# Performance work log

Hardware: AMD Instinct MI355X
Metric: run time of the kernel (lower is better)

## Reference

```python
import jax, jax.numpy as jnp
import numpy as np

D_MODEL = 1024
N_HEADS = 16
HEAD_DIM = D_MODEL // N_HEADS
D_FF = 4096
ROPE_BASE = 10000.0
LN_EPS = 1e-5


def setup_inputs() -> dict:
    key = jax.random.key(0)
    ks = jax.random.split(key, 12)
    B, S = 2, 2048
    s = 0.02
    inp = {
        "x": jax.random.normal(ks[0], (B, S, D_MODEL), dtype=jnp.float32),
        "Wq": jax.random.normal(ks[1], (D_MODEL, D_MODEL), dtype=jnp.float32) * s,
        "bq": jnp.zeros((D_MODEL,), jnp.float32),
        "Wk": jax.random.normal(ks[2], (D_MODEL, D_MODEL), dtype=jnp.float32) * s,
        "bk": jnp.zeros((D_MODEL,), jnp.float32),
        "Wv": jax.random.normal(ks[3], (D_MODEL, D_MODEL), dtype=jnp.float32) * s,
        "bv": jnp.zeros((D_MODEL,), jnp.float32),
        "Wo": jax.random.normal(ks[4], (D_MODEL, D_MODEL), dtype=jnp.float32) * s,
        "bo": jnp.zeros((D_MODEL,), jnp.float32),
        "ln1_g": jnp.ones((D_MODEL,), jnp.float32),
        "ln1_b": jnp.zeros((D_MODEL,), jnp.float32),
        "W1": jax.random.normal(ks[5], (D_MODEL, D_FF), dtype=jnp.float32) * s,
        "b1": jnp.zeros((D_FF,), jnp.float32),
        "W2": jax.random.normal(ks[6], (D_FF, D_MODEL), dtype=jnp.float32) * s,
        "b2": jnp.zeros((D_MODEL,), jnp.float32),
        "ln2_g": jnp.ones((D_MODEL,), jnp.float32),
        "ln2_b": jnp.zeros((D_MODEL,), jnp.float32),
    }
    return inp


def _layernorm(x, g, b):
    mu = jnp.mean(x, axis=-1, keepdims=True)
    var = jnp.var(x, axis=-1, keepdims=True)
    return (x - mu) * jax.lax.rsqrt(var + LN_EPS) * g + b


def _rope_cos_sin(seq_len, dtype):
    inv_freq = 1.0 / (ROPE_BASE ** (jnp.arange(0, HEAD_DIM, 2, dtype=jnp.float32) / HEAD_DIM))
    t = jnp.arange(seq_len, dtype=jnp.float32)
    freqs = jnp.einsum("i,j->ij", t, inv_freq)          # [S, HEAD_DIM/2]
    emb = jnp.concatenate([freqs, freqs], axis=-1)        # [S, HEAD_DIM]
    return jnp.cos(emb).astype(dtype), jnp.sin(emb).astype(dtype)


def _rotate_half(x):
    x1, x2 = jnp.split(x, 2, axis=-1)
    return jnp.concatenate([-x2, x1], axis=-1)


def reference(x, Wq, bq, Wk, bk, Wv, bv, Wo, bo, ln1_g, ln1_b,
              W1, b1, W2, b2, ln2_g, ln2_b):
    B, S, _ = x.shape
    residual = x
    h = _layernorm(x, ln1_g, ln1_b)

    def split_heads(y):  # [B,S,D] -> [B,H,S,hd]
        return y.reshape(B, S, N_HEADS, HEAD_DIM).transpose(0, 2, 1, 3)

    q = split_heads(h @ Wq + bq)
    k = split_heads(h @ Wk + bk)
    v = split_heads(h @ Wv + bv)

    cos, sin = _rope_cos_sin(S, x.dtype)  # [S, hd], broadcast over B,H
    q = q * cos + _rotate_half(q) * sin
    k = k * cos + _rotate_half(k) * sin

    scale = HEAD_DIM ** -0.5
    scores = jnp.einsum("bhqd,bhkd->bhqk", q, k) * scale
    attn = jax.nn.softmax(scores, axis=-1)
    ctx = jnp.einsum("bhqk,bhkd->bhqd", attn, v)           # [B,H,S,hd]
    ctx = ctx.transpose(0, 2, 1, 3).reshape(B, S, D_MODEL)
    attn_out = ctx @ Wo + bo

    x = residual + attn_out
    residual = x
    h = _layernorm(x, ln2_g, ln2_b)
    ffn = jax.nn.gelu(h @ W1 + b1, approximate=False) @ W2 + b2
    return residual + ffn
```

## Files before the change

kernel.cpp:

```cpp
#include <hip/hip_runtime.h>
#include <hip/hip_bf16.h>
#include <stdint.h>

#define S_LEN 2048
#define NH 16
#define HD 64
#define DM 1024
#define DFF 4096
#define MTOK 4096

typedef __attribute__((ext_vector_type(8))) short short8;
typedef __attribute__((ext_vector_type(4))) float f32x4;
typedef __attribute__((ext_vector_type(16))) float f32x16;
typedef __attribute__((ext_vector_type(2))) int i32x2;
typedef unsigned short u16;
typedef unsigned int u32;

__device__ __forceinline__ float bf2f(u16 u) {
  union { u32 i; float f; } x; x.i = ((u32)u) << 16; return x.f;
}
__device__ __forceinline__ u16 f2bf(float f) {
  union { float f; u32 i; } x; x.f = f;
  u32 r = x.i + 0x7fffu + ((x.i >> 16) & 1u);
  return (u16)(r >> 16);
}
__device__ __forceinline__ void gload16(const u16* g, u16* l) {
  __builtin_amdgcn_global_load_lds(
      (__attribute__((address_space(1))) u32*)g,
      (__attribute__((address_space(3))) u32*)l, 16, 0, 0);
}

#define VM0 asm volatile("s_waitcnt vmcnt(0)" ::: "memory")
#define VM6 asm volatile("s_waitcnt vmcnt(6)" ::: "memory")
#define BARR do { __builtin_amdgcn_s_barrier(); asm volatile("" ::: "memory"); } while (0)
#define LGKM0 do { asm volatile("s_waitcnt lgkmcnt(0)" ::: "memory"); __builtin_amdgcn_sched_barrier(0); } while (0)
#define PRIO1 __builtin_amdgcn_s_setprio(1)
#define PRIO0 __builtin_amdgcn_s_setprio(0)

__device__ __forceinline__ void transpose_tile(const float* __restrict__ W,
                                               u16* __restrict__ Wt, int K, int N,
                                               int n0, int k0, int tx, int ty,
                                               float (*tile)[33]) {
#pragma unroll
  for (int i = 0; i < 4; ++i)
    tile[ty + i * 8][tx] = W[(size_t)(k0 + ty + i * 8) * N + n0 + tx];
  __syncthreads();
#pragma unroll
  for (int i = 0; i < 4; ++i)
    Wt[(size_t)(n0 + ty + i * 8) * K + k0 + tx] = f2bf(tile[tx][ty + i * 8]);
}

__global__ __launch_bounds__(256) void prep(
    const float* __restrict__ Wq, const float* __restrict__ Wk,
    const float* __restrict__ Wv, const float* __restrict__ Wo,
    const float* __restrict__ W1, const float* __restrict__ W2,
    u16* __restrict__ WQKVT, u16* __restrict__ WOT, u16* __restrict__ W1T,
    u16* __restrict__ W2T, float* __restrict__ cosT, float* __restrict__ sinT,
    const float* __restrict__ x, const float* __restrict__ g,
    const float* __restrict__ b, u16* __restrict__ H) {
  __shared__ float tile[32][33];
  __shared__ float red[8];
  const int r = blockIdx.x;
  const int t = threadIdx.x;
  const int tx = t & 31, ty = t >> 5;
  if (r < 4096) {
    const float* W = (r < 1024) ? Wq : (r < 2048) ? Wk : (r < 3072) ? Wv : Wo;
    u16* Wt = (r < 1024) ? WQKVT
              : (r < 2048) ? WQKVT + 1024 * 1024
              : (r < 3072) ? WQKVT + 2 * 1024 * 1024 : WOT;
    int sub = r & 1023;
    transpose_tile(W, Wt, 1024, 1024, (sub & 31) * 32, (sub >> 5) * 32, tx, ty, tile);
  } else if (r < 8192) {
    int sub = r - 4096;
    transpose_tile(W1, W1T, 1024, 4096, (sub & 127) * 32, (sub >> 7) * 32, tx, ty, tile);
  } else if (r < 12288) {
    int sub = r - 8192;
    transpose_tile(W2, W2T, 4096, 1024, (sub & 31) * 32, (sub >> 5) * 32, tx, ty, tile);
  } else if (r < 12544) {
    int id = (r - 12288) * 256 + t;
    int s = id >> 5, j = id & 31;
    float inv = powf(10000.0f, -(float)j * (1.0f / 32.0f));
    float fr = (float)s * inv;
    cosT[id] = cosf(fr);
    sinT[id] = sinf(fr);
  } else {
    int row = r - 12544;
    float4 v = ((const float4*)(x + ((size_t)row << 10)))[t];
    float s = v.x + v.y + v.z + v.w;
    float q = v.x * v.x + v.y * v.y + v.z * v.z + v.w * v.w;
#pragma unroll
    for (int m = 1; m < 64; m <<= 1) {
      s += __shfl_xor(s, m, 64);
      q += __shfl_xor(q, m, 64);
    }
    int lane = t & 63, w = t >> 6;
    if (lane == 0) { red[w] = s; red[4 + w] = q; }
    __syncthreads();
    s = red[0] + red[1] + red[2] + red[3];
    q = red[4] + red[5] + red[6] + red[7];
    float mu = s * (1.0f / 1024.0f);
    float var = q * (1.0f / 1024.0f) - mu * mu;
    float rstd = rsqrtf(var + 1e-5f);
    float4 gv = ((const float4*)g)[t];
    float4 bv = ((const float4*)b)[t];
    ushort4 o;
    o.x = f2bf((v.x - mu) * rstd * gv.x + bv.x);
    o.y = f2bf((v.y - mu) * rstd * gv.y + bv.y);
    o.z = f2bf((v.z - mu) * rstd * gv.z + bv.z);
    o.w = f2bf((v.w - mu) * rstd * gv.w + bv.w);
    ((ushort4*)(H + ((size_t)row << 10)))[t] = o;
  }
}

__global__ __launch_bounds__(256) void ln_bf16(const float* __restrict__ x,
                                               const float* __restrict__ g,
                                               const float* __restrict__ b,
                                               u16* __restrict__ out) {
  int row = blockIdx.x;
  int t = threadIdx.x;
  float4 v = ((const float4*)(x + ((size_t)row << 10)))[t];
  float s = v.x + v.y + v.z + v.w;
  float q = v.x * v.x + v.y * v.y + v.z * v.z + v.w * v.w;
#pragma unroll
  for (int m = 1; m < 64; m <<= 1) {
    s += __shfl_xor(s, m, 64);
    q += __shfl_xor(q, m, 64);
  }
  __shared__ float red[8];
  int lane = t & 63, w = t >> 6;
  if (lane == 0) { red[w] = s; red[4 + w] = q; }
  __syncthreads();
  s = red[0] + red[1] + red[2] + red[3];
  q = red[4] + red[5] + red[6] + red[7];
  float mu = s * (1.0f / 1024.0f);
  float var = q * (1.0f / 1024.0f) - mu * mu;
  float rstd = rsqrtf(var + 1e-5f);
  float4 gv = ((const float4*)g)[t];
  float4 bv = ((const float4*)b)[t];
  ushort4 o;
  o.x = f2bf((v.x - mu) * rstd * gv.x + bv.x);
  o.y = f2bf((v.y - mu) * rstd * gv.y + bv.y);
  o.z = f2bf((v.z - mu) * rstd * gv.z + bv.z);
  o.w = f2bf((v.w - mu) * rstd * gv.w + bv.w);
  ((ushort4*)(out + ((size_t)row << 10)))[t] = o;
}

#define MMQ(IB, NB)                                                          \
  _Pragma("unroll") for (int i_ = 0; i_ < 4; ++i_)                           \
  _Pragma("unroll") for (int n_ = 0; n_ < 2; ++n_)                           \
  _Pragma("unroll") for (int k_ = 0; k_ < 2; ++k_)                           \
    acc[(IB) + i_][(NB) + n_] = __builtin_amdgcn_mfma_f32_16x16x32_bf16(     \
        a[i_][k_], b[(NB) + n_][k_], acc[(IB) + i_][(NB) + n_], 0, 0, 0);

template <int EPI>
__global__ __launch_bounds__(512, 2) void gemm256(
    const u16* __restrict__ A, const u16* __restrict__ Bt, int N, int K,
    const float* __restrict__ bias, const float* __restrict__ bq,
    const float* __restrict__ bk, const float* __restrict__ bv,
    const float* __restrict__ cosT, const float* __restrict__ sinT,
    u16* __restrict__ d0, u16* __restrict__ d1, u16* __restrict__ d2) {
  __shared__ __align__(16) u16 As[2][256 * 64];
  __shared__ __align__(16) u16 Bs[2][256 * 64];
  const int t = threadIdx.x;
  const int lane = t & 63, wid = t >> 6;
  const int fr = lane & 15, fq = lane >> 4;
  const int m0 = blockIdx.y << 8, n0 = blockIdx.x << 8;
  const int wmo = (wid >> 2) << 7;
  const int wno = (wid & 3) << 6;
  const int r7 = fr & 7;
  const int srow = t >> 3, ssl = t & 7;

  f32x4 acc[8][4];
#pragma unroll
  for (int i = 0; i < 8; ++i)
#pragma unroll
    for (int n = 0; n < 4; ++n) acc[i][n] = (f32x4){0.f, 0.f, 0.f, 0.f};

  short8 a[4][2], b[4][2];

  auto stageA = [&](int slot, int kt) {
#pragma unroll
    for (int c = 0; c < 4; ++c) {
      const int row = (c << 6) + srow;
      gload16(A + (size_t)(m0 + row) * K + kt + ((ssl ^ (row & 7)) << 3),
              &As[slot][(size_t)((c << 9) + t) << 3]);
    }
  };
  auto stageB = [&](int slot, int kt) {
#pragma unroll
    for (int c = 0; c < 4; ++c) {
      const int row = (c << 6) + srow;
      gload16(Bt + (size_t)(n0 + row) * K + kt + ((ssl ^ (row & 7)) << 3),
              &Bs[slot][(size_t)((c << 9) + t) << 3]);
    }
  };
  auto readA = [&](int slot, int ibase) {
#pragma unroll
    for (int i = 0; i < 4; ++i) {
      const u16* rp = &As[slot][(wmo + ((ibase + i) << 4) + fr) << 6];
      a[i][0] = *(const short8*)(rp + ((fq ^ r7) << 3));
      a[i][1] = *(const short8*)(rp + (((4 + fq) ^ r7) << 3));
    }
  };
  auto readB = [&](int slot, int nbase) {
#pragma unroll
    for (int n = 0; n < 2; ++n) {
      const u16* rp = &Bs[slot][(wno + ((nbase + n) << 4) + fr) << 6];
      b[nbase + n][0] = *(const short8*)(rp + ((fq ^ r7) << 3));
      b[nbase + n][1] = *(const short8*)(rp + (((4 + fq) ^ r7) << 3));
    }
  };

  stageA(0, 0);
  stageB(0, 0);
  const int iters = K >> 7;
  for (int it = 0; it < iters; ++it) {
    const int kt = it << 7;
    VM0; BARR;
    readA(0, 0); readB(0, 0);
    stageA(1, kt + 64);
    LGKM0; PRIO1; MMQ(0, 0); PRIO0;
    BARR;
    readB(0, 2);
    stageB(1, kt + 64);
    LGKM0; PRIO1; MMQ(0, 2); PRIO0;
    BARR;
    readA(0, 4);
    LGKM0; PRIO1; MMQ(4, 2); PRIO0;
    BARR;
    PRIO1; MMQ(4, 0); PRIO0;
    VM0; BARR;
    readA(1, 0); readB(1, 0);
    if (it + 1 < iters) stageA(0, kt + 128);
    LGKM0; PRIO1; MMQ(0, 0); PRIO0;
    BARR;
    readB(1, 2);
    if (it + 1 < iters) stageB(0, kt + 128);
    LGKM0; PRIO1; MMQ(0, 2); PRIO0;
    BARR;
    readA(1, 4);
    LGKM0; PRIO1; MMQ(4, 2); PRIO0;
    BARR;
    PRIO1; MMQ(4, 0); PRIO0;
  }

  if (EPI == 0) {
    const int colbase = n0 + wno;
    const int slice = colbase >> 10;
    const int cb = colbase & 1023;
    const int hh = cb >> 6;
    if (slice < 2) {
      const float sc = (slice == 0) ? 0.125f * 1.44269504088896f : 1.0f;
      const float* bb_ = (slice == 0) ? bq : bk;
      u16* dst = (slice == 0) ? d0 : d1;
#pragma unroll
      for (int i = 0; i < 8; ++i) {
        const int row0 = m0 + wmo + (i << 4) + (fq << 2);
#pragma unroll
        for (int n = 0; n < 2; ++n) {
          const int d = n * 16 + fr;
          const float blo = bb_[cb + d];
          const float bhi = bb_[cb + d + 32];
#pragma unroll
          for (int j = 0; j < 4; ++j) {
            const int row = row0 + j;
            const int ss = row & 2047, bb2 = row >> 11;
            const float c = cosT[ss * 32 + d];
            const float sn = sinT[ss * 32 + d];
            const float av = acc[i][n][j] + blo;
            const float bv2 = acc[i][n + 2][j] + bhi;
            const size_t base = ((size_t)((bb2 * 16 + hh) * 2048 + ss)) << 6;
            dst[base + d] = f2bf((av * c - bv2 * sn) * sc);
            dst[base + d + 32] = f2bf((bv2 * c + av * sn) * sc);
          }
        }
      }
    } else {
#pragma unroll
      for (int i = 0; i < 8; ++i) {
        const int row0 = m0 + wmo + (i << 4) + (fq << 2);
#pragma unroll
        for (int n = 0; n < 4; ++n) {
          const int d = n * 16 + fr;
          const float bia = bv[cb + d];
#pragma unroll
          for (int j = 0; j < 4; ++j) {
            const int row = row0 + j;
            const int ss = row & 2047, bb2 = row >> 11;
            d2[((size_t)((bb2 * 16 + hh) * 64 + d)) * 2048 + ss] =
                f2bf(acc[i][n][j] + bia);
          }
        }
      }
    }
  } else {
#pragma unroll
    for (int i = 0; i < 8; ++i) {
      const int row0 = m0 + wmo + (i << 4) + (fq << 2);
#pragma unroll
      for (int n = 0; n < 4; ++n) {
        const int col = n0 + wno + n * 16 + fr;
        const float bia = bias[col];
#pragma unroll
        for (int j = 0; j < 4; ++j) {
          const int row = row0 + j;
          const float v = acc[i][n][j] + bia;
          const float gl = 0.5f * v * (1.0f + erff(v * 0.70710678118f));
          d0[(size_t)row * N + col] = f2bf(gl);
        }
      }
    }
  }
}

__global__ __launch_bounds__(256, 2) void gemm_bt2(
    const u16* __restrict__ A, const u16* __restrict__ Bt, int K,
    const float* __restrict__ bias, const float* __restrict__ resid,
    float* __restrict__ dst) {
  __shared__ __align__(16) u16 As[3][128 * 64];
  __shared__ __align__(16) u16 Bs[3][64 * 64];
  const int t = threadIdx.x, lane = t & 63, wid = t >> 6;
  const int fr = lane & 15, fq = lane >> 4;
  const int bid = blockIdx.x;
  const int xcd = bid & 7, within = bid >> 3;
  const int m0 = (xcd * 4 + (within >> 4)) << 7;
  const int n0 = (within & 15) << 6;
  const int wm = (wid >> 1) << 6;
  const int wn = (wid & 1) << 5;
  const int sr = t >> 3, sl = t & 7;
  const int sw7 = fr & 7;

  f32x4 acc[4][2];
#pragma unroll
  for (int i = 0; i < 4; ++i)
#pragma unroll
    for (int n = 0; n < 2; ++n) acc[i][n] = (f32x4){0.f, 0.f, 0.f, 0.f};

  auto stage = [&](int b, int kt) {
#pragma unroll
    for (int c = 0; c < 4; ++c) {
      int R = c * 32 + sr;
      gload16(A + (size_t)(m0 + R) * K + kt + ((sl ^ (R & 7)) << 3),
              &As[b][R * 64 + sl * 8]);
    }
#pragma unroll
    for (int c = 0; c < 2; ++c) {
      int R = c * 32 + sr;
      gload16(Bt + (size_t)(n0 + R) * K + kt + ((sl ^ (R & 7)) << 3),
              &Bs[b][R * 64 + sl * 8]);
    }
  };

  stage(0, 0);
  stage(1, 64);
  const int iters = K >> 6;
  for (int it = 0; it < iters; ++it) {
    if (it + 1 < iters) { VM6; } else { VM0; }
    BARR;
    if (it + 2 < iters) stage((it + 2) % 3, (it + 2) << 6);
    const int slot = it % 3;
    short8 a[4][2], b[2][2];
#pragma unroll
    for (int i = 0; i < 4; ++i) {
      const char* rp = (const char*)&As[slot][(wm + i * 16 + fr) * 64];
      a[i][0] = *(const short8*)(rp + ((fq ^ sw7) << 4));
      a[i][1] = *(const short8*)(rp + (((4 + fq) ^ sw7) << 4));
    }
#pragma unroll
    for (int n = 0; n < 2; ++n) {
      const char* rp = (const char*)&Bs[slot][(wn + n * 16 + fr) * 64];
      b[n][0] = *(const short8*)(rp + ((fq ^ sw7) << 4));
      b[n][1] = *(const short8*)(rp + (((4 + fq) ^ sw7) << 4));
    }
    PRIO1;
#pragma unroll
    for (int i = 0; i < 4; ++i)
#pragma unroll
      for (int n = 0; n < 2; ++n)
#pragma unroll
        for (int k2 = 0; k2 < 2; ++k2)
          acc[i][n] = __builtin_amdgcn_mfma_f32_16x16x32_bf16(a[i][k2], b[n][k2],
                                                              acc[i][n], 0, 0, 0);
    PRIO0;
  }

#pragma unroll
  for (int i = 0; i < 4; ++i) {
    int row0 = m0 + wm + i * 16 + (fq << 2);
#pragma unroll
    for (int n = 0; n < 2; ++n) {
      int col = n0 + wn + n * 16 + fr;
      float bia = bias[col];
#pragma unroll
      for (int j = 0; j < 4; ++j) {
        size_t idx = (size_t)(row0 + j) * 1024 + col;
        dst[idx] = acc[i][n][j] + bia + resid[idx];
      }
    }
  }
}

__global__ __launch_bounds__(512, 4) void attn_fwd(const u16* __restrict__ q,
                                                   const u16* __restrict__ k,
                                                   const u16* __restrict__ vt,
                                                   u16* __restrict__ ctx) {
  __shared__ __align__(16) u16 Ks[2][2][64 * 64];
  __shared__ __align__(16) u16 Vs[2][2][64 * 64];
  __shared__ float Lr[4][32];
  const int t = threadIdx.x, lane = t & 63, w = t >> 6;
  const int qsub = w & 3, half = w >> 2;
  const int ql = lane & 31;
  const int h = lane >> 5;
  const int bid = blockIdx.x;
  const int bh = (bid & 7) * 4 + ((bid >> 3) & 3);
  const int qt = bid >> 5;
  const int q0w = qt * 128 + qsub * 32;
  const size_t hbase = (size_t)bh << 17;
  const u16* kg = k + hbase;
  const u16* vg = vt + hbase;
  const int srow = t >> 3;
  const int sl = t & 7;
  const int l7 = lane & 7;

  short8 qf[4];
#pragma unroll
  for (int f = 0; f < 4; ++f)
    qf[f] = *(const short8*)(q + hbase + (size_t)(q0w + ql) * 64 + f * 16 + h * 8);

  float lacc = 0.f;
  f32x16 o[2];
#pragma unroll
  for (int db = 0; db < 2; ++db)
#pragma unroll
    for (int r = 0; r < 16; ++r) o[db][r] = 0.f;

  auto stage = [&](int buf, int it1) {
    const int kt0 = it1 << 6;
    const int kt1 = (16 + it1) << 6;
    const int gs = sl ^ (srow & 7);
    gload16(kg + (size_t)(kt0 + srow) * 64 + gs * 8, &Ks[0][buf][srow * 64 + sl * 8]);
    gload16(kg + (size_t)(kt1 + srow) * 64 + gs * 8, &Ks[1][buf][srow * 64 + sl * 8]);
    gload16(vg + (size_t)srow * 2048 + kt0 + gs * 8, &Vs[0][buf][srow * 64 + sl * 8]);
    gload16(vg + (size_t)srow * 2048 + kt1 + gs * 8, &Vs[1][buf][srow * 64 + sl * 8]);
  };

  stage(0, 0);
  int buf = 0;
  for (int it = 0; it < 16; ++it) {
    VM0;
    BARR;
    if (it < 15) stage(buf ^ 1, it + 1);

    f32x16 s[2];
    PRIO1;
#pragma unroll
    for (int kb = 0; kb < 2; ++kb) {
#pragma unroll
      for (int r = 0; r < 16; ++r) s[kb][r] = 0.f;
#pragma unroll
      for (int f = 0; f < 4; ++f) {
        const u16* kr = &Ks[half][buf][(kb * 32 + ql) * 64 + (((2 * f + h) ^ l7) << 3)];
        s[kb] = __builtin_amdgcn_mfma_f32_32x32x16_bf16(*(const short8*)kr, qf[f],
                                                        s[kb], 0, 0, 0);
      }
    }
    PRIO0;

    float p[2][16];
#pragma unroll
    for (int kb = 0; kb < 2; ++kb)
#pragma unroll
      for (int r = 0; r < 16; ++r) {
        p[kb][r] = exp2f(s[kb][r]);
        lacc += p[kb][r];
      }

    short8 pf[4];
#pragma unroll
    for (int kb = 0; kb < 2; ++kb)
#pragma unroll
      for (int rrp = 0; rrp < 2; ++rrp) {
        u32 y0, y1, x0, x1;
        asm volatile("v_cvt_pk_bf16_f32 %0, %1, %2" : "=v"(y0)
                     : "v"(p[kb][8 * rrp + 0]), "v"(p[kb][8 * rrp + 1]));
        asm volatile("v_cvt_pk_bf16_f32 %0, %1, %2" : "=v"(y1)
                     : "v"(p[kb][8 * rrp + 2]), "v"(p[kb][8 * rrp + 3]));
        asm volatile("v_cvt_pk_bf16_f32 %0, %1, %2" : "=v"(x0)
                     : "v"(p[kb][8 * rrp + 4]), "v"(p[kb][8 * rrp + 5]));
        asm volatile("v_cvt_pk_bf16_f32 %0, %1, %2" : "=v"(x1)
                     : "v"(p[kb][8 * rrp + 6]), "v"(p[kb][8 * rrp + 7]));
        i32x2 r0 = __builtin_amdgcn_permlane32_swap((int)x0, (int)y0, false, false);
        i32x2 r1 = __builtin_amdgcn_permlane32_swap((int)x1, (int)y1, false, false);
        u32 dw[4] = {(u32)r0[1], (u32)r1[1], (u32)r0[0], (u32)r1[0]};
        pf[kb * 2 + rrp] = *(short8*)dw;
      }

    PRIO1;
#pragma unroll
    for (int db = 0; db < 2; ++db) {
#pragma unroll
      for (int f = 0; f < 4; ++f) {
        const u16* vr = &Vs[half][buf][(db * 32 + ql) * 64 + (((2 * f + h) ^ l7) << 3)];
        o[db] = __builtin_amdgcn_mfma_f32_32x32x16_bf16(pf[f], *(const short8*)vr,
                                                        o[db], 0, 0, 0);
      }
    }
    PRIO0;
    buf ^= 1;
  }

  lacc += __shfl_xor(lacc, 32, 64);

  BARR;
  float* mO = (float*)&Ks[0][0][0];
  float* mL = (float*)&Vs[0][0][0];
  if (half == 1) {
#pragma unroll
    for (int r = 0; r < 16; ++r) {
      const int qr = (r & 3) + 8 * (r >> 2) + 4 * h;
#pragma unroll
      for (int db = 0; db < 2; ++db)
        mO[(qsub * 32 + qr) * 64 + db * 32 + ql] = o[db][r];
    }
    if (h == 0) mL[qsub * 32 + ql] = lacc;
  }
  LGKM0;
  BARR;
  if (half == 0) {
    float lsum = lacc + mL[qsub * 32 + ql];
    Lr[qsub][ql] = 1.0f / lsum;
#pragma unroll
    for (int r = 0; r < 16; ++r) {
      const int qr = (r & 3) + 8 * (r >> 2) + 4 * h;
#pragma unroll
      for (int db = 0; db < 2; ++db)
        o[db][r] += mO[(qsub * 32 + qr) * 64 + db * 32 + ql];
    }
    LGKM0;
    const int bb = bh >> 4, hh = bh & 15;
#pragma unroll
    for (int r = 0; r < 16; ++r) {
      const int qr = (r & 3) + 8 * (r >> 2) + 4 * h;
      const float rl = Lr[qsub][qr];
      const int row = q0w + qr;
      const size_t base = (((size_t)(bb * 2048 + row)) << 10) + hh * 64;
#pragma unroll
      for (int db = 0; db < 2; ++db)
        ctx[base + db * 32 + ql] = f2bf(o[db][r] * rl);
    }
  }
}

extern "C" void kernel_launch(void* const* d_in, const int* in_sizes, int n_in,
                              void* d_out, int out_size, void* d_ws, size_t ws_size,
                              hipStream_t stream) {
  const float* x    = (const float*)d_in[0];
  const float* Wq   = (const float*)d_in[1];
  const float* bq   = (const float*)d_in[2];
  const float* Wk   = (const float*)d_in[3];
  const float* bk   = (const float*)d_in[4];
  const float* Wv   = (const float*)d_in[5];
  const float* bv   = (const float*)d_in[6];
  const float* Wo   = (const float*)d_in[7];
  const float* bo   = (const float*)d_in[8];
  const float* ln1g = (const float*)d_in[9];
  const float* ln1b = (const float*)d_in[10];
  const float* W1   = (const float*)d_in[11];
  const float* b1   = (const float*)d_in[12];
  const float* W2   = (const float*)d_in[13];
  const float* b2   = (const float*)d_in[14];
  const float* ln2g = (const float*)d_in[15];
  const float* ln2b = (const float*)d_in[16];

  char* ws = (char*)d_ws;
  size_t off = 0;
  auto alloc = [&](size_t bytes) {
    char* p = ws + off;
    off += (bytes + 1023) & ~(size_t)1023;
    return p;
  };
  u16* WQKVT = (u16*)alloc((size_t)3 * DM * DM * 2);
  u16* WOT = (u16*)alloc((size_t)DM * DM * 2);
  u16* W1T = (u16*)alloc((size_t)DFF * DM * 2);
  u16* W2T = (u16*)alloc((size_t)DM * DFF * 2);
  float* COS = (float*)alloc((size_t)S_LEN * 32 * 4);
  float* SIN = (float*)alloc((size_t)S_LEN * 32 * 4);
  u16* H   = (u16*)alloc((size_t)MTOK * DM * 2);
  u16* Qb  = (u16*)alloc((size_t)MTOK * DM * 2);
  u16* Kb  = (u16*)alloc((size_t)MTOK * DM * 2);
  u16* VT  = (u16*)alloc((size_t)MTOK * DM * 2);
  u16* CTX = (u16*)alloc((size_t)MTOK * DM * 2);
  float* X2 = (float*)alloc((size_t)MTOK * DM * 4);
  u16* FFN1 = Qb;
  if (ws_size < off) return;

  dim3 blk256(256);
  prep<<<dim3(16640), blk256, 0, stream>>>(Wq, Wk, Wv, Wo, W1, W2, WQKVT, WOT,
                                           W1T, W2T, COS, SIN, x, ln1g, ln1b, H);
  gemm256<0><<<dim3(12, 16), dim3(512), 0, stream>>>(
      H, WQKVT, 3072, 1024, nullptr, bq, bk, bv, COS, SIN, Qb, Kb, VT);
  attn_fwd<<<dim3(512), dim3(512), 0, stream>>>(Qb, Kb, VT, CTX);
  gemm_bt2<<<dim3(512), blk256, 0, stream>>>(CTX, WOT, 1024, bo, x, X2);
  ln_bf16<<<4096, blk256, 0, stream>>>(X2, ln2g, ln2b, H);
  gemm256<1><<<dim3(16, 16), dim3(512), 0, stream>>>(
      H, W1T, 4096, 1024, b1, nullptr, nullptr, nullptr, nullptr, nullptr,
      FFN1, nullptr, nullptr);
  gemm_bt2<<<dim3(512), blk256, 0, stream>>>(FFN1, W2T, 4096, b2, X2, (float*)d_out);
}
```

Before: 241.6 us.

## Replace output GEMMs with 128x128-tile intra-block split-K kernel

Replaces the 128x64-tile, 256-thread, triple-buffered GEMM used for the Wo and W2 projections with a 128x128-tile, 512-thread kernel. It splits each 128-wide K step between two groups of four waves and merges their partial sums through LDS before the bias+residual epilogue. The larger tile is meant to raise operand reuse and halve the grid. The cost is that only 256 blocks are launched, buffering drops to two stages with a full vmcnt(0) wait each iteration, the 128 KB LDS footprint limits occupancy to one block per CU, and the epilogue adds an LDS reduction.

```diff
diff --git a/kernel.cpp b/kernel.cpp
--- a/kernel.cpp
+++ b/kernel.cpp
@@ -31,7 +31,6 @@
 }
 
 #define VM0 asm volatile("s_waitcnt vmcnt(0)" ::: "memory")
-#define VM6 asm volatile("s_waitcnt vmcnt(6)" ::: "memory")
 #define BARR do { __builtin_amdgcn_s_barrier(); asm volatile("" ::: "memory"); } while (0)
 #define LGKM0 do { asm volatile("s_waitcnt lgkmcnt(0)" ::: "memory"); __builtin_amdgcn_sched_barrier(0); } while (0)
 #define PRIO1 __builtin_amdgcn_s_setprio(1)
@@ -313,88 +312,111 @@
   }
 }
 
-__global__ __launch_bounds__(256, 2) void gemm_bt2(
+__global__ __launch_bounds__(512, 1) void gemm_split(
     const u16* __restrict__ A, const u16* __restrict__ Bt, int K,
     const float* __restrict__ bias, const float* __restrict__ resid,
     float* __restrict__ dst) {
-  __shared__ __align__(16) u16 As[3][128 * 64];
-  __shared__ __align__(16) u16 Bs[3][64 * 64];
-  const int t = threadIdx.x, lane = t & 63, wid = t >> 6;
+  __shared__ __align__(16) u16 As[2][128 * 128];
+  __shared__ __align__(16) u16 Bs[2][128 * 128];
+  const int t = threadIdx.x, lane = t & 63, w = t >> 6;
   const int fr = lane & 15, fq = lane >> 4;
+  const int wq = w & 3, kh = w >> 2;
+  const int wm = (wq >> 1) << 6, wn = (wq & 1) << 6;
   const int bid = blockIdx.x;
   const int xcd = bid & 7, within = bid >> 3;
-  const int m0 = (xcd * 4 + (within >> 4)) << 7;
-  const int n0 = (within & 15) << 6;
-  const int wm = (wid >> 1) << 6;
-  const int wn = (wid & 1) << 5;
-  const int sr = t >> 3, sl = t & 7;
-  const int sw7 = fr & 7;
-
-  f32x4 acc[4][2];
+  const int m0 = (xcd * 4 + (within >> 3)) << 7;
+  const int n0 = (within & 7) << 7;
+  const int srow = t >> 4;
+  const int ssl = t & 15;
+
+  f32x4 acc[4][4];
 #pragma unroll
   for (int i = 0; i < 4; ++i)
 #pragma unroll
-    for (int n = 0; n < 2; ++n) acc[i][n] = (f32x4){0.f, 0.f, 0.f, 0.f};
-
-  auto stage = [&](int b, int kt) {
+    for (int n = 0; n < 4; ++n) acc[i][n] = (f32x4){0.f, 0.f, 0.f, 0.f};
+
+  auto stage = [&](int buf, int kt) {
 #pragma unroll
     for (int c = 0; c < 4; ++c) {
-      int R = c * 32 + sr;
-      gload16(A + (size_t)(m0 + R) * K + kt + ((sl ^ (R & 7)) << 3),
-              &As[b][R * 64 + sl * 8]);
-    }
-#pragma unroll
-    for (int c = 0; c < 2; ++c) {
-      int R = c * 32 + sr;
-      gload16(Bt + (size_t)(n0 + R) * K + kt + ((sl ^ (R & 7)) << 3),
-              &Bs[b][R * 64 + sl * 8]);
+      const int R = c * 32 + srow;
+      const int gs = ssl ^ (R & 15);
+      gload16(A + (size_t)(m0 + R) * K + kt + gs * 8, &As[buf][R * 128 + ssl * 8]);
+    }
+#pragma unroll
+    for (int c = 0; c < 4; ++c) {
+      const int R = c * 32 + srow;
+      const int gs = ssl ^ (R & 15);
+      gload16(Bt + (size_t)(n0 + R) * K + kt + gs * 8, &Bs[buf][R * 128 + ssl * 8]);
     }
   };
 
   stage(0, 0);
-  stage(1, 64);
-  const int iters = K >> 6;
+  int buf = 0;
+  const int iters = K >> 7;
   for (int it = 0; it < iters; ++it) {
-    if (it + 1 < iters) { VM6; } else { VM0; }
-    BARR;
-    if (it + 2 < iters) stage((it + 2) % 3, (it + 2) << 6);
-    const int slot = it % 3;
-    short8 a[4][2], b[2][2];
+    VM0;
+    BARR;
+    if (it + 1 < iters) stage(buf ^ 1, (it + 1) << 7);
+
+    short8 a[4][2], b[4][2];
 #pragma unroll
     for (int i = 0; i < 4; ++i) {
-      const char* rp = (const char*)&As[slot][(wm + i * 16 + fr) * 64];
-      a[i][0] = *(const short8*)(rp + ((fq ^ sw7) << 4));
-      a[i][1] = *(const short8*)(rp + (((4 + fq) ^ sw7) << 4));
-    }
-#pragma unroll
-    for (int n = 0; n < 2; ++n) {
-      const char* rp = (const char*)&Bs[slot][(wn + n * 16 + fr) * 64];
-      b[n][0] = *(const short8*)(rp + ((fq ^ sw7) << 4));
-      b[n][1] = *(const short8*)(rp + (((4 + fq) ^ sw7) << 4));
+      const u16* rp = &As[buf][(wm + i * 16 + fr) * 128];
+#pragma unroll
+      for (int ks = 0; ks < 2; ++ks)
+        a[i][ks] = *(const short8*)(rp + (((kh * 8 + ks * 4 + fq) ^ fr) << 3));
+    }
+#pragma unroll
+    for (int n = 0; n < 4; ++n) {
+      const u16* rp = &Bs[buf][(wn + n * 16 + fr) * 128];
+#pragma unroll
+      for (int ks = 0; ks < 2; ++ks)
+        b[n][ks] = *(const short8*)(rp + (((kh * 8 + ks * 4 + fq) ^ fr) << 3));
     }
     PRIO1;
 #pragma unroll
     for (int i = 0; i < 4; ++i)
 #pragma unroll
-      for (int n = 0; n < 2; ++n)
-#pragma unroll
-        for (int k2 = 0; k2 < 2; ++k2)
-          acc[i][n] = __builtin_amdgcn_mfma_f32_16x16x32_bf16(a[i][k2], b[n][k2],
+      for (int n = 0; n < 4; ++n)
+#pragma unroll
+        for (int ks = 0; ks < 2; ++ks)
+          acc[i][n] = __builtin_amdgcn_mfma_f32_16x16x32_bf16(a[i][ks], b[n][ks],
                                                               acc[i][n], 0, 0, 0);
     PRIO0;
-  }
-
-#pragma unroll
-  for (int i = 0; i < 4; ++i) {
-    int row0 = m0 + wm + i * 16 + (fq << 2);
-#pragma unroll
-    for (int n = 0; n < 2; ++n) {
-      int col = n0 + wn + n * 16 + fr;
-      float bia = bias[col];
-#pragma unroll
-      for (int j = 0; j < 4; ++j) {
-        size_t idx = (size_t)(row0 + j) * 1024 + col;
-        dst[idx] = acc[i][n][j] + bia + resid[idx];
+    buf ^= 1;
+  }
+
+  BARR;
+  float* mrg = (float*)&As[0][0];
+  if (kh == 1) {
+#pragma unroll
+    for (int i = 0; i < 4; ++i) {
+      const int ri = i * 16 + (fq << 2);
+#pragma unroll
+      for (int n = 0; n < 4; ++n) {
+        const int ci = n * 16 + fr;
+        *(f32x4*)(mrg + wq * 4352 + ci * 68 + ri) = acc[i][n];
+      }
+    }
+  }
+  LGKM0;
+  BARR;
+  if (kh == 0) {
+#pragma unroll
+    for (int i = 0; i < 4; ++i) {
+      const int ri = i * 16 + (fq << 2);
+      const int row0 = m0 + wm + ri;
+#pragma unroll
+      for (int n = 0; n < 4; ++n) {
+        const int ci = n * 16 + fr;
+        const int col = n0 + wn + ci;
+        const f32x4 other = *(const f32x4*)(mrg + wq * 4352 + ci * 68 + ri);
+        const float bia = bias[col];
+#pragma unroll
+        for (int j = 0; j < 4; ++j) {
+          size_t idx = (size_t)(row0 + j) * 1024 + col;
+          dst[idx] = acc[i][n][j] + other[j] + bia + resid[idx];
+        }
       }
     }
   }
@@ -600,10 +622,10 @@
   gemm256<0><<<dim3(12, 16), dim3(512), 0, stream>>>(
       H, WQKVT, 3072, 1024, nullptr, bq, bk, bv, COS, SIN, Qb, Kb, VT);
   attn_fwd<<<dim3(512), dim3(512), 0, stream>>>(Qb, Kb, VT, CTX);
-  gemm_bt2<<<dim3(512), blk256, 0, stream>>>(CTX, WOT, 1024, bo, x, X2);
+  gemm_split<<<dim3(256), dim3(512), 0, stream>>>(CTX, WOT, 1024, bo, x, X2);
   ln_bf16<<<4096, blk256, 0, stream>>>(X2, ln2g, ln2b, H);
   gemm256<1><<<dim3(16, 16), dim3(512), 0, stream>>>(
       H, W1T, 4096, 1024, b1, nullptr, nullptr, nullptr, nullptr, nullptr,
       FFN1, nullptr, nullptr);
-  gemm_bt2<<<dim3(512), blk256, 0, stream>>>(FFN1, W2T, 4096, b2, X2, (float*)d_out);
-}
+  gemm_split<<<dim3(256), dim3(512), 0, stream>>>(FFN1, W2T, 4096, b2, X2, (float*)d_out);
+}
```

After: 233.3 us. -3.4%, faster.
